# Performance work log

Hardware: AMD Instinct MI355X
Metric: run time of the kernel (lower is better)

The kernel has to match this reference:

```python
import jax, jax.numpy as jnp
import numpy as np
from jax.scipy.special import logsumexp

IN_FEATURES = 1024
N_CLASSES = 50257
CUTOFFS = [4000, 20000, N_CLASSES]  # includes final n_classes, as in the module
SHORTLIST = CUTOFFS[0]
N_CLUSTERS = len(CUTOFFS)
N = 8192


def setup_inputs() -> dict:
    key = jax.random.key(0)
    k1, k2, k3, k4, k5, k6 = jax.random.split(key, 6)
    inp = {
        "input": jax.random.normal(k1, (N, IN_FEATURES), dtype=jnp.float32),
        "target": jax.random.randint(k2, (N,), 0, N_CLASSES, dtype=jnp.int64)
        if jax.config.jax_enable_x64 else jax.random.randint(k2, (N,), 0, N_CLASSES, dtype=jnp.int32),
        # learned parameters
        "weight": jax.random.normal(k3, (N_CLASSES, IN_FEATURES), dtype=jnp.float32) * 0.02,
        "bias": jnp.zeros((N_CLASSES,), dtype=jnp.float32),
        "tail_vectors": jax.random.normal(k4, (N_CLUSTERS - 1, IN_FEATURES), dtype=jnp.float32) * 0.02,
        "tail_bias": jnp.zeros((N_CLUSTERS - 1,), dtype=jnp.float32),
    }
    return inp


def reference(input, target, weight, bias, tail_vectors, tail_bias):
    cutoff_values = [0] + CUTOFFS  # [0, 4000, 20000, 50257]

    # head = shortlist classes + one logit per tail cluster
    head_weight = jnp.concatenate([weight[:SHORTLIST], tail_vectors], axis=0)
    head_bias = jnp.concatenate([bias[:SHORTLIST], tail_bias], axis=0)
    head_logits = input @ head_weight.T + head_bias              # [N, shortlist + n_clusters-1]
    head_logprob = jax.nn.log_softmax(head_logits, axis=1)

    # which cluster each target falls in: 0 = shortlist, 1.. = tails
    boundaries = jnp.asarray(CUTOFFS[:-1])                        # [4000, 20000]
    cluster_id = jnp.searchsorted(boundaries, target, side="right")  # [N]

    # index into head distribution: target itself for shortlist, else cluster logit slot
    gather_inds = jnp.where(cluster_id == 0, target, SHORTLIST + cluster_id - 1)
    head_term = jnp.take_along_axis(head_logprob, gather_inds[:, None], axis=1)[:, 0]

    # per-row target logit against the full table (only used for tail rows)
    target_logit = jnp.sum(input * weight[target], axis=-1) + bias[target]  # [N]

    # tail clusters: within-cluster log-prob of the target = logit - logsumexp(cluster logits)
    tail_term = jnp.zeros_like(head_term)
    for i in range(1, N_CLUSTERS):
        lo, hi = cutoff_values[i], cutoff_values[i + 1]
        cluster_logits = input @ weight[lo:hi].T + bias[lo:hi]    # [N, hi-lo]
        lse = logsumexp(cluster_logits, axis=1)                   # [N]
        tail_term = jnp.where(cluster_id == i, target_logit - lse, tail_term)

    output = head_term + tail_term                                # [N] log-probs of targets
    loss = jnp.mean(-output)
    return output, loss
```

## Files before the change

kernel.cpp:

```cpp
#include <hip/hip_runtime.h>
#include <stddef.h>
#include <stdint.h>

#define IN_F      1024
#define SHORTLIST 4000
#define C1_LO     4000
#define C1_HI     20000
#define C2_HI     50257
#define NROWS     8192

#define WS_CNT1   0
#define WS_CNT2   1
#define WS_LOSS   2
#define WS_RL1    4
#define WS_RL2    (4 + 8192)
#define WS_SEH    (4 + 2*8192)
#define WS_SET    (WS_SEH + 8192)
#define WS_CAP    (WS_SET + 8192)
#define WS_WORDS  (WS_CAP + 8192)

#define WBF_OFF   (262144)
#define WBF_BYTES ((size_t)C2_HI * IN_F * 2)
#define XBF_OFF   (WBF_OFF + 103219200)
#define XBF_BYTES ((size_t)NROWS * IN_F * 2)
#define WS_NEEDED (XBF_OFF + XBF_BYTES)

typedef float          f32x4  __attribute__((ext_vector_type(4)));
typedef __bf16         bf16x8 __attribute__((ext_vector_type(8)));
typedef unsigned short us8    __attribute__((ext_vector_type(8)));
typedef unsigned short ushort_t;

__device__ __forceinline__ unsigned short f2bf(float f) {
    unsigned int u = __float_as_uint(f);
    u += 0x7fffu + ((u >> 16) & 1u);
    return (unsigned short)(u >> 16);
}

__device__ __forceinline__ void gl_lds16(const void* g, void* l) {
    __builtin_amdgcn_global_load_lds(
        (const __attribute__((address_space(1))) void*)g,
        (__attribute__((address_space(3))) void*)l, 16, 0, 0);
}

__global__ void init_ws_k(int* __restrict__ ws) {
    int i = blockIdx.x * 256 + threadIdx.x;
    if (i < WS_WORDS) {
        int v = (i >= WS_RL1 && i < WS_RL1 + 2*8192) ? -1 : 0;
        ws[i] = v;
    }
}

__global__ void compact_rows_k(const int* __restrict__ target, int* __restrict__ ws) {
    int row = blockIdx.x * 256 + threadIdx.x;
    if (row >= NROWS) return;
    int tg = target[row];
    if (tg >= C1_LO) {
        if (tg < C1_HI) {
            int p = atomicAdd(&ws[WS_CNT1], 1);
            ws[WS_RL1 + p] = row;
        } else {
            int p = atomicAdd(&ws[WS_CNT2], 1);
            ws[WS_RL2 + p] = row;
        }
    }
}

__global__ void convert_bf16_k(const float* __restrict__ src,
                               ushort_t* __restrict__ dst, int nchunks) {
    int i = blockIdx.x * 256 + threadIdx.x;
    if (i >= nchunks) return;
    const float* p = src + (size_t)i * 8;
    f32x4 x0 = *(const f32x4*)p;
    f32x4 x1 = *(const f32x4*)(p + 4);
    us8 o;
    o[0] = f2bf(x0[0]); o[1] = f2bf(x0[1]); o[2] = f2bf(x0[2]); o[3] = f2bf(x0[3]);
    o[4] = f2bf(x1[0]); o[5] = f2bf(x1[1]); o[6] = f2bf(x1[2]); o[7] = f2bf(x1[3]);
    *(us8*)(dst + (size_t)i * 8) = o;
}

__launch_bounds__(256)
__global__ void gemm_lse_bf16_k(const ushort_t* __restrict__ Xbf,
                                const ushort_t* __restrict__ Wbf,
                                const float* __restrict__ bias,
                                const int*   __restrict__ target,
                                const int*   __restrict__ rowlist,
                                const int*   __restrict__ cnt_ptr,
                                int fixed_cnt,
                                int class_base, int C,
                                float* __restrict__ sumexp,
                                float* __restrict__ capture)
{
    const int cnt = cnt_ptr ? *cnt_ptr : fixed_cnt;
    const int r0  = blockIdx.x * 128;
    if (r0 >= cnt) return;
    const int c0  = blockIdx.y * 128;

    __shared__ ushort_t As[128 * 64];
    __shared__ ushort_t Bs[128 * 64];
    __shared__ int   orig_s[128];
    __shared__ int   tgt_s[128];
    __shared__ float bias_s[128];

    const int tid = threadIdx.x;
    if (tid < 128) {
        int idx  = r0 + tid;
        int orig = (idx < cnt) ? (rowlist ? rowlist[idx] : idx) : -1;
        orig_s[tid] = orig;
        tgt_s[tid]  = (orig >= 0) ? target[orig] : -1;
        int c = c0 + tid;
        bias_s[tid] = (c < C) ? bias[class_base + c] : 0.f;
    }
    __syncthreads();

    const int lane = tid & 63;
    const int wave = tid >> 6;
    const int wm = wave >> 1, wn = wave & 1;
    const int q = lane >> 4, s = lane & 15;

    const int lrow  = lane >> 3;
    const int chunk = (lane & 7) ^ lrow;
    const ushort_t* aptr[4];
    const ushort_t* bptr[4];
    ushort_t* alds[4];
    ushort_t* blds[4];
#pragma unroll
    for (int i = 0; i < 4; ++i) {
        int t  = wave * 4 + i;
        int rt = t * 8 + lrow;
        int orig = orig_s[rt]; if (orig < 0) orig = 0;
        aptr[i] = Xbf + (size_t)orig * IN_F + chunk * 8;
        int c = c0 + rt; if (c >= C) c = C - 1;
        bptr[i] = Wbf + (size_t)(class_base + c) * IN_F + chunk * 8;
        alds[i] = &As[t * 512];
        blds[i] = &Bs[t * 512];
    }

    int aoff[4], boff[4];
#pragma unroll
    for (int i = 0; i < 4; ++i) {
        aoff[i] = (wm * 64 + i * 16 + s) * 64;
        boff[i] = (wn * 64 + i * 16 + s) * 64;
    }
    const int slot0 = (q ^ (s & 7)) * 8;
    const int slot1 = slot0 ^ (4 * 8);

    f32x4 acc[4][4];
#pragma unroll
    for (int mi = 0; mi < 4; ++mi)
#pragma unroll
        for (int ni = 0; ni < 4; ++ni) acc[mi][ni] = (f32x4)0.f;

    for (int k0 = 0; k0 < IN_F; k0 += 64) {
        __syncthreads();
#pragma unroll
        for (int i = 0; i < 4; ++i) {
            gl_lds16(aptr[i] + k0, alds[i]);
            gl_lds16(bptr[i] + k0, blds[i]);
        }
        __syncthreads();

#pragma unroll
        for (int ks = 0; ks < 2; ++ks) {
            const int sl = ks ? slot1 : slot0;
            bf16x8 av[4], bv[4];
#pragma unroll
            for (int i = 0; i < 4; ++i) {
                av[i] = *(const bf16x8*)&As[aoff[i] + sl];
                bv[i] = *(const bf16x8*)&Bs[boff[i] + sl];
            }
#pragma unroll
            for (int mi = 0; mi < 4; ++mi)
#pragma unroll
                for (int ni = 0; ni < 4; ++ni)
                    acc[mi][ni] = __builtin_amdgcn_mfma_f32_16x16x32_bf16(
                        av[mi], bv[ni], acc[mi][ni], 0, 0, 0);
        }
    }

#pragma unroll
    for (int mi = 0; mi < 4; ++mi) {
#pragma unroll
        for (int r = 0; r < 4; ++r) {
            int rl   = wm * 64 + mi * 16 + q * 4 + r;
            int orig = orig_s[rl];
            int tg   = tgt_s[rl];
            float sum = 0.f;
#pragma unroll
            for (int ni = 0; ni < 4; ++ni) {
                int cl = wn * 64 + ni * 16 + s;
                int cg = c0 + cl;
                float logit = acc[mi][ni][r] + bias_s[cl];
                bool valid = (cg < C) && (orig >= 0);
                float e = valid ? __expf(logit) : 0.f;
                sum += e;
                if (valid && (class_base + cg == tg)) capture[orig] = logit;
            }
            sum += __shfl_xor(sum, 1, 64);
            sum += __shfl_xor(sum, 2, 64);
            sum += __shfl_xor(sum, 4, 64);
            sum += __shfl_xor(sum, 8, 64);
            if (s == 0 && orig >= 0) atomicAdd(&sumexp[orig], sum);
        }
    }
}

__launch_bounds__(256)
__global__ void gemm_lse_k(const float* __restrict__ input,
                           const float* __restrict__ weight,
                           const float* __restrict__ bias,
                           const int*   __restrict__ target,
                           const int*   __restrict__ rowlist,
                           const int*   __restrict__ cnt_ptr,
                           int fixed_cnt,
                           int class_base, int C,
                           float* __restrict__ sumexp,
                           float* __restrict__ capture)
{
    const int cnt = cnt_ptr ? *cnt_ptr : fixed_cnt;
    const int r0  = blockIdx.x * 128;
    if (r0 >= cnt) return;
    const int c0  = blockIdx.y * 128;

    __shared__ unsigned short As[128 * 40];
    __shared__ unsigned short Bs[128 * 40];
    __shared__ int   orig_s[128];
    __shared__ int   tgt_s[128];
    __shared__ float bias_s[128];

    const int tid = threadIdx.x;
    if (tid < 128) {
        int idx  = r0 + tid;
        int orig = -1;
        if (idx < cnt) orig = rowlist ? rowlist[idx] : idx;
        orig_s[tid] = orig;
        tgt_s[tid]  = (orig >= 0) ? target[orig] : -1;
        int c = c0 + tid;
        bias_s[tid] = (c < C) ? bias[class_base + c] : 0.f;
    }

    const int lane = tid & 63;
    const int wave = tid >> 6;
    const int wm = wave >> 1, wn = wave & 1;
    const int q = lane >> 4, s = lane & 15;

    int aoff[4], boff[4];
#pragma unroll
    for (int i = 0; i < 4; ++i) {
        aoff[i] = (wm * 64 + i * 16 + s) * 40 + q * 8;
        boff[i] = (wn * 64 + i * 16 + s) * 40 + q * 8;
    }

    f32x4 acc[4][4];
#pragma unroll
    for (int mi = 0; mi < 4; ++mi)
#pragma unroll
        for (int ni = 0; ni < 4; ++ni) acc[mi][ni] = (f32x4)0.f;

    for (int k0 = 0; k0 < IN_F; k0 += 32) {
        __syncthreads();
#pragma unroll
        for (int i = 0; i < 2; ++i) {
            int sg  = tid + i * 256;
            int row = sg >> 2;
            int sk  = (sg & 3) << 3;
            {
                int orig = orig_s[row];
                float v[8];
                if (orig >= 0) {
                    const float* p = input + (size_t)orig * IN_F + k0 + sk;
                    f32x4 x0 = *(const f32x4*)p;
                    f32x4 x1 = *(const f32x4*)(p + 4);
                    v[0]=x0[0]; v[1]=x0[1]; v[2]=x0[2]; v[3]=x0[3];
                    v[4]=x1[0]; v[5]=x1[1]; v[6]=x1[2]; v[7]=x1[3];
                } else {
#pragma unroll
                    for (int j = 0; j < 8; ++j) v[j] = 0.f;
                }
                us8 o;
#pragma unroll
                for (int j = 0; j < 8; ++j) o[j] = f2bf(v[j]);
                *(us8*)&As[row * 40 + sk] = o;
            }
            {
                int c = c0 + row;
                float v[8];
                if (c < C) {
                    const float* p = weight + (size_t)(class_base + c) * IN_F + k0 + sk;
                    f32x4 x0 = *(const f32x4*)p;
                    f32x4 x1 = *(const f32x4*)(p + 4);
                    v[0]=x0[0]; v[1]=x0[1]; v[2]=x0[2]; v[3]=x0[3];
                    v[4]=x1[0]; v[5]=x1[1]; v[6]=x1[2]; v[7]=x1[3];
                } else {
#pragma unroll
                    for (int j = 0; j < 8; ++j) v[j] = 0.f;
                }
                us8 o;
#pragma unroll
                for (int j = 0; j < 8; ++j) o[j] = f2bf(v[j]);
                *(us8*)&Bs[row * 40 + sk] = o;
            }
        }
        __syncthreads();

        bf16x8 av[4], bv[4];
#pragma unroll
        for (int i = 0; i < 4; ++i) {
            av[i] = *(const bf16x8*)&As[aoff[i]];
            bv[i] = *(const bf16x8*)&Bs[boff[i]];
        }
#pragma unroll
        for (int mi = 0; mi < 4; ++mi)
#pragma unroll
            for (int ni = 0; ni < 4; ++ni)
                acc[mi][ni] = __builtin_amdgcn_mfma_f32_16x16x32_bf16(
                    av[mi], bv[ni], acc[mi][ni], 0, 0, 0);
    }

#pragma unroll
    for (int mi = 0; mi < 4; ++mi) {
#pragma unroll
        for (int r = 0; r < 4; ++r) {
            int rl   = wm * 64 + mi * 16 + q * 4 + r;
            int orig = orig_s[rl];
            int tg   = tgt_s[rl];
            float sum = 0.f;
#pragma unroll
            for (int ni = 0; ni < 4; ++ni) {
                int cl = wn * 64 + ni * 16 + s;
                int cg = c0 + cl;
                float logit = acc[mi][ni][r] + bias_s[cl];
                bool valid = (cg < C) && (orig >= 0);
                float e = valid ? __expf(logit) : 0.f;
                sum += e;
                if (valid && (class_base + cg == tg)) capture[orig] = logit;
            }
            sum += __shfl_xor(sum, 1, 64);
            sum += __shfl_xor(sum, 2, 64);
            sum += __shfl_xor(sum, 4, 64);
            sum += __shfl_xor(sum, 8, 64);
            if (s == 0 && orig >= 0) atomicAdd(&sumexp[orig], sum);
        }
    }
}

__global__ void combine_k(const float* __restrict__ input,
                          const int*   __restrict__ target,
                          const float* __restrict__ tv,
                          const float* __restrict__ tb,
                          const float* __restrict__ sumexp_head,
                          const float* __restrict__ sumexp_tail,
                          const float* __restrict__ capture,
                          float* __restrict__ out,
                          float* __restrict__ loss_accum)
{
    const int wave = threadIdx.x >> 6, lane = threadIdx.x & 63;
    const int row = blockIdx.x * 4 + wave;
    if (row >= NROWS) return;

    const float* x  = input + (size_t)row * IN_F + lane * 16;
    const float* p0 = tv + lane * 16;
    const float* p1 = tv + IN_F + lane * 16;
    float d0 = 0.f, d1 = 0.f;
#pragma unroll
    for (int i = 0; i < 16; i += 4) {
        f32x4 xv = *(const f32x4*)(x  + i);
        f32x4 a  = *(const f32x4*)(p0 + i);
        f32x4 b  = *(const f32x4*)(p1 + i);
        d0 += xv[0]*a[0] + xv[1]*a[1] + xv[2]*a[2] + xv[3]*a[3];
        d1 += xv[0]*b[0] + xv[1]*b[1] + xv[2]*b[2] + xv[3]*b[3];
    }
#pragma unroll
    for (int m = 32; m; m >>= 1) {
        d0 += __shfl_xor(d0, m, 64);
        d1 += __shfl_xor(d1, m, 64);
    }
    if (lane == 0) {
        float t0 = d0 + tb[0];
        float t1 = d1 + tb[1];
        int tg  = target[row];
        int cid = (tg < C1_LO) ? 0 : ((tg < C1_HI) ? 1 : 2);
        float se_head  = sumexp_head[row] + __expf(t0) + __expf(t1);
        float lse_head = __logf(se_head);
        float head_num = (cid == 0) ? capture[row] : ((cid == 1) ? t0 : t1);
        float o = head_num - lse_head;
        if (cid != 0) o += capture[row] - __logf(sumexp_tail[row]);
        out[row] = o;
        atomicAdd(loss_accum, o);
    }
}

__global__ void finalize_k(const float* __restrict__ loss_accum, float* __restrict__ out) {
    out[NROWS] = -loss_accum[0] * (1.0f / NROWS);
}

extern "C" void kernel_launch(void* const* d_in, const int* in_sizes, int n_in,
                              void* d_out, int out_size, void* d_ws, size_t ws_size,
                              hipStream_t stream) {
    const float* input  = (const float*)d_in[0];
    const int*   target = (const int*)  d_in[1];
    const float* weight = (const float*)d_in[2];
    const float* bias   = (const float*)d_in[3];
    const float* tv     = (const float*)d_in[4];
    const float* tb     = (const float*)d_in[5];
    float* out = (float*)d_out;
    int*   wsI = (int*)d_ws;
    float* wsF = (float*)d_ws;

    init_ws_k<<<dim3((WS_WORDS + 255) / 256), 256, 0, stream>>>(wsI);
    compact_rows_k<<<dim3(NROWS / 256), 256, 0, stream>>>(target, wsI);

    const bool fast = ws_size >= (size_t)WS_NEEDED;

    if (fast) {
        ushort_t* Wbf = (ushort_t*)((char*)d_ws + WBF_OFF);
        ushort_t* Xbf = (ushort_t*)((char*)d_ws + XBF_OFF);

        const int wchunks = (C2_HI * IN_F) / 8;
        const int xchunks = (NROWS * IN_F) / 8;
        convert_bf16_k<<<dim3((wchunks + 255) / 256), 256, 0, stream>>>(weight, Wbf, wchunks);
        convert_bf16_k<<<dim3((xchunks + 255) / 256), 256, 0, stream>>>(input, Xbf, xchunks);

        gemm_lse_bf16_k<<<dim3(NROWS / 128, (SHORTLIST + 127) / 128), 256, 0, stream>>>(
            Xbf, Wbf, bias, target,
            nullptr, nullptr, NROWS,
            0, SHORTLIST,
            wsF + WS_SEH, wsF + WS_CAP);

        gemm_lse_bf16_k<<<dim3(NROWS / 128, (C1_HI - C1_LO) / 128), 256, 0, stream>>>(
            Xbf, Wbf, bias, target,
            wsI + WS_RL1, wsI + WS_CNT1, 0,
            C1_LO, C1_HI - C1_LO,
            wsF + WS_SET, wsF + WS_CAP);

        gemm_lse_bf16_k<<<dim3(NROWS / 128, (C2_HI - C1_HI + 127) / 128), 256, 0, stream>>>(
            Xbf, Wbf, bias, target,
            wsI + WS_RL2, wsI + WS_CNT2, 0,
            C1_HI, C2_HI - C1_HI,
            wsF + WS_SET, wsF + WS_CAP);
    } else {
        gemm_lse_k<<<dim3(NROWS / 128, (SHORTLIST + 127) / 128), 256, 0, stream>>>(
            input, weight, bias, target,
            nullptr, nullptr, NROWS,
            0, SHORTLIST,
            wsF + WS_SEH, wsF + WS_CAP);
        gemm_lse_k<<<dim3(NROWS / 128, (C1_HI - C1_LO) / 128), 256, 0, stream>>>(
            input, weight, bias, target,
            wsI + WS_RL1, wsI + WS_CNT1, 0,
            C1_LO, C1_HI - C1_LO,
            wsF + WS_SET, wsF + WS_CAP);
        gemm_lse_k<<<dim3(NROWS / 128, (C2_HI - C1_HI + 127) / 128), 256, 0, stream>>>(
            input, weight, bias, target,
            wsI + WS_RL2, wsI + WS_CNT2, 0,
            C1_HI, C2_HI - C1_HI,
            wsF + WS_SET, wsF + WS_CAP);
    }

    combine_k<<<dim3(NROWS / 4), 256, 0, stream>>>(
        input, target, tv, tb,
        wsF + WS_SEH, wsF + WS_SET, wsF + WS_CAP,
        out, wsF + WS_LOSS);

    finalize_k<<<1, 1, 0, stream>>>(wsF + WS_LOSS, out);
}
```

Baseline: 1.443 ms.

## Fuse three cluster GEMM-LSE launches into one grid with per-block column loop

Merges the two bf16 conversion launches into one kernel and replaces the three per-cluster GEMM+logsumexp launches with a single flattened grid in which block ranges map to head, tail1 and tail2. Each block now loops over four 128-column tiles, accumulating exp sums in shared memory and issuing one atomic per row instead of one per tile. This cuts launch count, tail-wave idle time between kernels and global atomic traffic. In exchange, blocks for tail clusters whose row count is small exit early and leave grid slots empty, and the A tile is reloaded per column tile rather than being kept resident.

New measurement: 1.439 ms. No clear change (-0.3%).

```diff
diff --git a/kernel.cpp b/kernel.cpp
--- a/kernel.cpp
+++ b/kernel.cpp
@@ -20,10 +20,14 @@
 #define WS_WORDS  (WS_CAP + 8192)
 
 #define WBF_OFF   (262144)
-#define WBF_BYTES ((size_t)C2_HI * IN_F * 2)
 #define XBF_OFF   (WBF_OFF + 103219200)
 #define XBF_BYTES ((size_t)NROWS * IN_F * 2)
 #define WS_NEEDED (XBF_OFF + XBF_BYTES)
+
+#define GRID_HEAD 512
+#define GRID_T1   2048
+#define GRID_T2   3840
+#define GRID_ALL  (GRID_HEAD + GRID_T1 + GRID_T2)
 
 typedef float          f32x4  __attribute__((ext_vector_type(4)));
 typedef __bf16         bf16x8 __attribute__((ext_vector_type(8)));
@@ -65,50 +69,73 @@
     }
 }
 
-__global__ void convert_bf16_k(const float* __restrict__ src,
-                               ushort_t* __restrict__ dst, int nchunks) {
+#define WCHUNKS ((C2_HI * IN_F) / 8)
+#define XCHUNKS ((NROWS * IN_F) / 8)
+__global__ void convert_bf16_k(const float* __restrict__ w_src,
+                               ushort_t* __restrict__ w_dst,
+                               const float* __restrict__ x_src,
+                               ushort_t* __restrict__ x_dst) {
     int i = blockIdx.x * 256 + threadIdx.x;
-    if (i >= nchunks) return;
-    const float* p = src + (size_t)i * 8;
+    const float* p;
+    ushort_t* d;
+    if (i < WCHUNKS) { p = w_src + (size_t)i * 8; d = w_dst + (size_t)i * 8; }
+    else {
+        int j = i - WCHUNKS;
+        if (j >= XCHUNKS) return;
+        p = x_src + (size_t)j * 8; d = x_dst + (size_t)j * 8;
+    }
     f32x4 x0 = *(const f32x4*)p;
     f32x4 x1 = *(const f32x4*)(p + 4);
     us8 o;
     o[0] = f2bf(x0[0]); o[1] = f2bf(x0[1]); o[2] = f2bf(x0[2]); o[3] = f2bf(x0[3]);
     o[4] = f2bf(x1[0]); o[5] = f2bf(x1[1]); o[6] = f2bf(x1[2]); o[7] = f2bf(x1[3]);
-    *(us8*)(dst + (size_t)i * 8) = o;
+    *(us8*)d = o;
 }
 
 __launch_bounds__(256)
-__global__ void gemm_lse_bf16_k(const ushort_t* __restrict__ Xbf,
-                                const ushort_t* __restrict__ Wbf,
-                                const float* __restrict__ bias,
-                                const int*   __restrict__ target,
-                                const int*   __restrict__ rowlist,
-                                const int*   __restrict__ cnt_ptr,
-                                int fixed_cnt,
-                                int class_base, int C,
-                                float* __restrict__ sumexp,
-                                float* __restrict__ capture)
+__global__ void gemm_lse_fused_k(const ushort_t* __restrict__ Xbf,
+                                 const ushort_t* __restrict__ Wbf,
+                                 const float* __restrict__ bias,
+                                 const int*   __restrict__ target,
+                                 int*   __restrict__ wsI,
+                                 float* __restrict__ wsF)
 {
-    const int cnt = cnt_ptr ? *cnt_ptr : fixed_cnt;
-    const int r0  = blockIdx.x * 128;
+    const int bid = blockIdx.x;
+    int rs, cg, cbase, C, cnt;
+    const int* rowlist;
+    float* sumexp;
+    if (bid < GRID_HEAD) {
+        rs = bid & 63; cg = bid >> 6;
+        cbase = 0; C = SHORTLIST; rowlist = nullptr; cnt = NROWS;
+        sumexp = wsF + WS_SEH;
+    } else if (bid < GRID_HEAD + GRID_T1) {
+        int b = bid - GRID_HEAD;
+        rs = b & 63; cg = b >> 6;
+        cbase = C1_LO; C = C1_HI - C1_LO; rowlist = wsI + WS_RL1; cnt = wsI[WS_CNT1];
+        sumexp = wsF + WS_SET;
+    } else {
+        int b = bid - (GRID_HEAD + GRID_T1);
+        rs = b & 63; cg = b >> 6;
+        cbase = C1_HI; C = C2_HI - C1_HI; rowlist = wsI + WS_RL2; cnt = wsI[WS_CNT2];
+        sumexp = wsF + WS_SET;
+    }
+    const int r0 = rs * 128;
     if (r0 >= cnt) return;
-    const int c0  = blockIdx.y * 128;
+    float* capture = wsF + WS_CAP;
 
     __shared__ ushort_t As[128 * 64];
     __shared__ ushort_t Bs[128 * 64];
     __shared__ int   orig_s[128];
     __shared__ int   tgt_s[128];
-    __shared__ float bias_s[128];
+    __shared__ float part[256];
 
     const int tid = threadIdx.x;
+    part[tid] = 0.f;
     if (tid < 128) {
         int idx  = r0 + tid;
         int orig = (idx < cnt) ? (rowlist ? rowlist[idx] : idx) : -1;
         orig_s[tid] = orig;
         tgt_s[tid]  = (orig >= 0) ? target[orig] : -1;
-        int c = c0 + tid;
-        bias_s[tid] = (c < C) ? bias[class_base + c] : 0.f;
     }
     __syncthreads();
 
@@ -120,19 +147,18 @@
     const int lrow  = lane >> 3;
     const int chunk = (lane & 7) ^ lrow;
     const ushort_t* aptr[4];
-    const ushort_t* bptr[4];
     ushort_t* alds[4];
     ushort_t* blds[4];
+    int brow[4];
 #pragma unroll
     for (int i = 0; i < 4; ++i) {
         int t  = wave * 4 + i;
         int rt = t * 8 + lrow;
         int orig = orig_s[rt]; if (orig < 0) orig = 0;
         aptr[i] = Xbf + (size_t)orig * IN_F + chunk * 8;
-        int c = c0 + rt; if (c >= C) c = C - 1;
-        bptr[i] = Wbf + (size_t)(class_base + c) * IN_F + chunk * 8;
         alds[i] = &As[t * 512];
         blds[i] = &Bs[t * 512];
+        brow[i] = rt;
     }
 
     int aoff[4], boff[4];
@@ -144,62 +170,88 @@
     const int slot0 = (q ^ (s & 7)) * 8;
     const int slot1 = slot0 ^ (4 * 8);
 
-    f32x4 acc[4][4];
-#pragma unroll
-    for (int mi = 0; mi < 4; ++mi)
-#pragma unroll
-        for (int ni = 0; ni < 4; ++ni) acc[mi][ni] = (f32x4)0.f;
-
-    for (int k0 = 0; k0 < IN_F; k0 += 64) {
-        __syncthreads();
+    for (int ct = 0; ct < 4; ++ct) {
+        const int c0 = (cg * 4 + ct) * 128;
+        if (c0 >= C) break;
+
+        const ushort_t* bptr[4];
 #pragma unroll
         for (int i = 0; i < 4; ++i) {
-            gl_lds16(aptr[i] + k0, alds[i]);
-            gl_lds16(bptr[i] + k0, blds[i]);
-        }
-        __syncthreads();
-
-#pragma unroll
-        for (int ks = 0; ks < 2; ++ks) {
-            const int sl = ks ? slot1 : slot0;
-            bf16x8 av[4], bv[4];
+            int c = c0 + brow[i]; if (c >= C) c = C - 1;
+            bptr[i] = Wbf + (size_t)(cbase + c) * IN_F + chunk * 8;
+        }
+
+        f32x4 acc[4][4];
+#pragma unroll
+        for (int mi = 0; mi < 4; ++mi)
+#pragma unroll
+            for (int ni = 0; ni < 4; ++ni) acc[mi][ni] = (f32x4)0.f;
+
+        for (int k0 = 0; k0 < IN_F; k0 += 64) {
+            __syncthreads();
 #pragma unroll
             for (int i = 0; i < 4; ++i) {
-                av[i] = *(const bf16x8*)&As[aoff[i] + sl];
-                bv[i] = *(const bf16x8*)&Bs[boff[i] + sl];
-            }
-#pragma unroll
-            for (int mi = 0; mi < 4; ++mi)
-#pragma unroll
-                for (int ni = 0; ni < 4; ++ni)
-                    acc[mi][ni] = __builtin_amdgcn_mfma_f32_16x16x32_bf16(
-                        av[mi], bv[ni], acc[mi][ni], 0, 0, 0);
-        }
-    }
-
-#pragma unroll
-    for (int mi = 0; mi < 4; ++mi) {
-#pragma unroll
-        for (int r = 0; r < 4; ++r) {
-            int rl   = wm * 64 + mi * 16 + q * 4 + r;
-            int orig = orig_s[rl];
-            int tg   = tgt_s[rl];
-            float sum = 0.f;
-#pragma unroll
-            for (int ni = 0; ni < 4; ++ni) {
-                int cl = wn * 64 + ni * 16 + s;
-                int cg = c0 + cl;
-                float logit = acc[mi][ni][r] + bias_s[cl];
-                bool valid = (cg < C) && (orig >= 0);
-                float e = valid ? __expf(logit) : 0.f;
-                sum += e;
-                if (valid && (class_base + cg == tg)) capture[orig] = logit;
-            }
-            sum += __shfl_xor(sum, 1, 64);
-            sum += __shfl_xor(sum, 2, 64);
-            sum += __shfl_xor(sum, 4, 64);
-            sum += __shfl_xor(sum, 8, 64);
-            if (s == 0 && orig >= 0) atomicAdd(&sumexp[orig], sum);
+                gl_lds16(aptr[i] + k0, alds[i]);
+                gl_lds16(bptr[i] + k0, blds[i]);
+            }
+            __syncthreads();
+
+#pragma unroll
+            for (int ks = 0; ks < 2; ++ks) {
+                const int sl = ks ? slot1 : slot0;
+                bf16x8 av[4], bv[4];
+#pragma unroll
+                for (int i = 0; i < 4; ++i) {
+                    av[i] = *(const bf16x8*)&As[aoff[i] + sl];
+                    bv[i] = *(const bf16x8*)&Bs[boff[i] + sl];
+                }
+#pragma unroll
+                for (int mi = 0; mi < 4; ++mi)
+#pragma unroll
+                    for (int ni = 0; ni < 4; ++ni)
+                        acc[mi][ni] = __builtin_amdgcn_mfma_f32_16x16x32_bf16(
+                            av[mi], bv[ni], acc[mi][ni], 0, 0, 0);
+            }
+        }
+
+        float bias_v[4];
+#pragma unroll
+        for (int ni = 0; ni < 4; ++ni) {
+            int cgl = c0 + wn * 64 + ni * 16 + s;
+            bias_v[ni] = (cgl < C) ? bias[cbase + cgl] : 0.f;
+        }
+#pragma unroll
+        for (int mi = 0; mi < 4; ++mi) {
+#pragma unroll
+            for (int r = 0; r < 4; ++r) {
+                int rl   = wm * 64 + mi * 16 + q * 4 + r;
+                int orig = orig_s[rl];
+                int tg   = tgt_s[rl];
+                float sum = 0.f;
+#pragma unroll
+                for (int ni = 0; ni < 4; ++ni) {
+                    int cgl = c0 + wn * 64 + ni * 16 + s;
+                    float logit = acc[mi][ni][r] + bias_v[ni];
+                    bool valid = (cgl < C) && (orig >= 0);
+                    float e = valid ? __expf(logit) : 0.f;
+                    sum += e;
+                    if (valid && (cbase + cgl == tg)) capture[orig] = logit;
+                }
+                sum += __shfl_xor(sum, 1, 64);
+                sum += __shfl_xor(sum, 2, 64);
+                sum += __shfl_xor(sum, 4, 64);
+                sum += __shfl_xor(sum, 8, 64);
+                if (s == 0 && orig >= 0) part[wn * 128 + rl] += sum;
+            }
+        }
+    }
+
+    __syncthreads();
+    if (tid < 128) {
+        int orig = orig_s[tid];
+        if (orig >= 0) {
+            float tot = part[tid] + part[128 + tid];
+            atomicAdd(&sumexp[orig], tot);
         }
     }
 }
@@ -415,35 +467,18 @@
         ushort_t* Wbf = (ushort_t*)((char*)d_ws + WBF_OFF);
         ushort_t* Xbf = (ushort_t*)((char*)d_ws + XBF_OFF);
 
-        const int wchunks = (C2_HI * IN_F) / 8;
-        const int xchunks = (NROWS * IN_F) / 8;
-        convert_bf16_k<<<dim3((wchunks + 255) / 256), 256, 0, stream>>>(weight, Wbf, wchunks);
-        convert_bf16_k<<<dim3((xchunks + 255) / 256), 256, 0, stream>>>(input, Xbf, xchunks);
-
-        gemm_lse_bf16_k<<<dim3(NROWS / 128, (SHORTLIST + 127) / 128), 256, 0, stream>>>(
-            Xbf, Wbf, bias, target,
-            nullptr, nullptr, NROWS,
-            0, SHORTLIST,
-            wsF + WS_SEH, wsF + WS_CAP);
-
-        gemm_lse_bf16_k<<<dim3(NROWS / 128, (C1_HI - C1_LO) / 128), 256, 0, stream>>>(
-            Xbf, Wbf, bias, target,
-            wsI + WS_RL1, wsI + WS_CNT1, 0,
-            C1_LO, C1_HI - C1_LO,
-            wsF + WS_SET, wsF + WS_CAP);
-
-        gemm_lse_bf16_k<<<dim3(NROWS / 128, (C2_HI - C1_HI + 127) / 128), 256, 0, stream>>>(
-            Xbf, Wbf, bias, target,
-            wsI + WS_RL2, wsI + WS_CNT2, 0,
-            C1_HI, C2_HI - C1_HI,
-            wsF + WS_SET, wsF + WS_CAP);
+        convert_bf16_k<<<dim3((WCHUNKS + XCHUNKS + 255) / 256), 256, 0, stream>>>(
+            weight, Wbf, input, Xbf);
+
+        gemm_lse_fused_k<<<dim3(GRID_ALL), 256, 0, stream>>>(
+            Xbf, Wbf, bias, target, wsI, wsF);
     } else {
         gemm_lse_k<<<dim3(NROWS / 128, (SHORTLIST + 127) / 128), 256, 0, stream>>>(
             input, weight, bias, target,
             nullptr, nullptr, NROWS,
             0, SHORTLIST,
             wsF + WS_SEH, wsF + WS_CAP);
-        gemm_lse_k<<<dim3(NROWS / 128, (C1_HI - C1_LO) / 128), 256, 0, stream>>>(
+        gemm_lse_k<<<dim3(NROWS / 128, (C1_HI - C1_LO + 127) / 128), 256, 0, stream>>>(
             input, weight, bias, target,
             wsI + WS_RL1, wsI + WS_CNT1, 0,
             C1_LO, C1_HI - C1_LO,
```
